# Performance work log

Hardware: AMD Instinct MI355X
Metric: run time of the kernel (lower is better)

Reference implementation:

```python
import jax, jax.numpy as jnp
import numpy as np

N_NODES = 100000
N_EDGES = 1600000
N_FEAT = 64
DIM = 32
N_CLASSES = 10
N_GRAPHS = 64
BN_EPS = 1e-5


def setup_inputs() -> dict:
    key = jax.random.key(0)
    ks = jax.random.split(key, 20)
    x = jax.random.normal(ks[0], (N_NODES, N_FEAT), dtype=jnp.float32)
    edge_index = jax.random.randint(ks[1], (2, N_EDGES), 0, N_NODES, dtype=jnp.int64)
    batch = jnp.sort(jax.random.randint(ks[2], (N_NODES,), 0, N_GRAPHS, dtype=jnp.int64))
    s = 0.1
    # conv1 MLP (in=N_FEAT)
    w1a = jax.random.normal(ks[3], (N_FEAT, DIM), dtype=jnp.float32) * s
    b1a = jnp.zeros((DIM,), jnp.float32)
    w1b = jax.random.normal(ks[4], (DIM, DIM), dtype=jnp.float32) * s
    b1b = jnp.zeros((DIM,), jnp.float32)
    # convs 2-5 MLPs stacked [4, DIM, DIM]
    Wa = jax.random.normal(ks[5], (4, DIM, DIM), dtype=jnp.float32) * s
    Ba = jnp.zeros((4, DIM), jnp.float32)
    Wb = jax.random.normal(ks[6], (4, DIM, DIM), dtype=jnp.float32) * s
    Bb = jnp.zeros((4, DIM), jnp.float32)
    bn_gamma = jnp.ones((5, DIM), jnp.float32)
    bn_beta = jnp.zeros((5, DIM), jnp.float32)
    fc1_w = jax.random.normal(ks[7], (DIM, DIM), dtype=jnp.float32) * s
    fc1_b = jnp.zeros((DIM,), jnp.float32)
    fc2_w = jax.random.normal(ks[8], (DIM, N_CLASSES), dtype=jnp.float32) * s
    fc2_b = jnp.zeros((N_CLASSES,), jnp.float32)
    return dict(x=x, edge_index=edge_index, batch=batch,
                w1a=w1a, b1a=b1a, w1b=w1b, b1b=b1b,
                Wa=Wa, Ba=Ba, Wb=Wb, Bb=Bb,
                bn_gamma=bn_gamma, bn_beta=bn_beta,
                fc1_w=fc1_w, fc1_b=fc1_b, fc2_w=fc2_w, fc2_b=fc2_b)


def _gin_aggr(x, src, dst):
    # sum_{j in N(i)} x_j  + x_i   (eps = 0)
    agg = jax.ops.segment_sum(x[src], dst, num_segments=N_NODES)
    return x + agg


def _mlp(h, wa, ba, wb, bb):
    return jax.nn.relu(h @ wa + ba) @ wb + bb


def _bn(h, gamma, beta):
    mu = jnp.mean(h, axis=0)
    var = jnp.mean((h - mu) ** 2, axis=0)  # biased, torch BN training mode
    return (h - mu) * jax.lax.rsqrt(var + BN_EPS) * gamma + beta


def reference(x, edge_index, batch, w1a, b1a, w1b, b1b, Wa, Ba, Wb, Bb,
              bn_gamma, bn_beta, fc1_w, fc1_b, fc2_w, fc2_b):
    src, dst = edge_index[0], edge_index[1]
    # layer 1 (num_features -> dim)
    h = _mlp(_gin_aggr(x, src, dst), w1a, b1a, w1b, b1b)
    h = _bn(jax.nn.relu(h), bn_gamma[0], bn_beta[0])
    # layers 2-5 (dim -> dim)
    for i in range(4):
        h = _mlp(_gin_aggr(h, src, dst), Wa[i], Ba[i], Wb[i], Bb[i])
        h = _bn(jax.nn.relu(h), bn_gamma[i + 1], bn_beta[i + 1])
    # global add pool over graphs
    g = jax.ops.segment_sum(h, batch, num_segments=N_GRAPHS)  # [G, dim]
    g = jax.nn.relu(g @ fc1_w + fc1_b)
    # dropout: eval mode -> identity
    return g @ fc2_w + fc2_b  # [G, num_classes]
```

## Files before the change

kernel.cpp:

```cpp
#include <hip/hip_runtime.h>
#include <hip/hip_fp16.h>

#define NN 100000
#define NE 1600000
#define NF 64
#define DM 32
#define NG 64
#define NC 10
#define BN_EPS 1e-5f

#define BSHIFT 8
#define NBUCK ((NN + 255) >> 8)
#define CHUNK 8192
#define NCH ((NE + CHUNK - 1) / CHUNK)

__device__ __forceinline__ float2 up2(unsigned u) {
    __half2 h = __builtin_bit_cast(__half2, u);
    return __half22float2(h);
}
__device__ __forceinline__ unsigned pk2(float a, float b) {
    __half2 h = __floats2half2_rn(a, b);
    return __builtin_bit_cast(unsigned, h);
}
__device__ __forceinline__ void acc8(float* a, uint4 w) {
    float2 p;
    p = up2(w.x); a[0] += p.x; a[1] += p.y;
    p = up2(w.y); a[2] += p.x; a[3] += p.y;
    p = up2(w.z); a[4] += p.x; a[5] += p.y;
    p = up2(w.w); a[6] += p.x; a[7] += p.y;
}

__global__ __launch_bounds__(256) void binA_k(const int* __restrict__ ei,
                                              int* __restrict__ bcnt) {
    __shared__ int h[NBUCK];
    for (int i = threadIdx.x; i < NBUCK; i += 256) h[i] = 0;
    __syncthreads();
    long long base = (long long)blockIdx.x * CHUNK;
    int n = (int)((NE - base < CHUNK) ? (NE - base) : CHUNK);
    for (int i = threadIdx.x; i < n; i += 256) {
        int d = ei[NE + base + i];
        atomicAdd(&h[d >> BSHIFT], 1);
    }
    __syncthreads();
    for (int i = threadIdx.x; i < NBUCK; i += 256)
        if (h[i]) atomicAdd(&bcnt[i], h[i]);
}

__global__ __launch_bounds__(512) void binB_k(const int* __restrict__ bcnt,
                                              int* __restrict__ bbase,
                                              int* __restrict__ bcur) {
    __shared__ int s[512];
    int t = threadIdx.x;
    int v = (t < NBUCK) ? bcnt[t] : 0;
    s[t] = v;
    __syncthreads();
    int acc = v;
    for (int off = 1; off < 512; off <<= 1) {
        int add = (t >= off) ? s[t - off] : 0;
        __syncthreads();
        acc += add;
        s[t] = acc;
        __syncthreads();
    }
    if (t < NBUCK) { bbase[t] = acc - v; bcur[t] = acc - v; }
    if (t == 0) bbase[NBUCK] = NE;
}

__global__ __launch_bounds__(256) void binC_k(const int* __restrict__ ei,
                                              int* __restrict__ bcur,
                                              unsigned* __restrict__ binned) {
    __shared__ int cnt[NBUCK];
    __shared__ int ofs[NBUCK];
    __shared__ int idx[NBUCK];
    for (int i = threadIdx.x; i < NBUCK; i += 256) { cnt[i] = 0; idx[i] = 0; }
    __syncthreads();
    long long base = (long long)blockIdx.x * CHUNK;
    int n = (int)((NE - base < CHUNK) ? (NE - base) : CHUNK);
    int d[CHUNK / 256];
#pragma unroll
    for (int k = 0; k < CHUNK / 256; k++) {
        int i = threadIdx.x + k * 256;
        int dd = (i < n) ? ei[NE + base + i] : -1;
        d[k] = dd;
        if (dd >= 0) atomicAdd(&cnt[dd >> BSHIFT], 1);
    }
    __syncthreads();
    for (int i = threadIdx.x; i < NBUCK; i += 256)
        if (cnt[i]) ofs[i] = atomicAdd(&bcur[i], cnt[i]);
    __syncthreads();
#pragma unroll
    for (int k = 0; k < CHUNK / 256; k++) {
        int i = threadIdx.x + k * 256;
        if (i < n) {
            unsigned src = (unsigned)ei[base + i];
            int b = d[k] >> BSHIFT;
            int l = atomicAdd(&idx[b], 1);
            binned[ofs[b] + l] = (src << 8) | (unsigned)(d[k] & 255);
        }
    }
}

__global__ __launch_bounds__(256) void binD_k(const unsigned* __restrict__ binned,
                                              const int* __restrict__ bbase,
                                              int* __restrict__ rowptr,
                                              int* __restrict__ csr) {
    __shared__ int cnt[256];
    __shared__ int cur[256];
    __shared__ int s[256];
    int b = blockIdx.x;
    int e0 = bbase[b], e1 = bbase[b + 1];
    int t = threadIdx.x;
    cnt[t] = 0;
    __syncthreads();
    for (int e = e0 + t; e < e1; e += 256) atomicAdd(&cnt[binned[e] & 255u], 1);
    __syncthreads();
    int v = cnt[t];
    s[t] = v;
    __syncthreads();
    int acc = v;
    for (int off = 1; off < 256; off <<= 1) {
        int add = (t >= off) ? s[t - off] : 0;
        __syncthreads();
        acc += add;
        s[t] = acc;
        __syncthreads();
    }
    int base = e0 + acc - v;
    int node = (b << BSHIFT) + t;
    if (node < NN) rowptr[node] = base;
    cur[t] = base;
    if (b == NBUCK - 1 && t == 0) rowptr[NN] = NE;
    __syncthreads();
    for (int e = e0 + t; e < e1; e += 256) {
        unsigned w = binned[e];
        int p = atomicAdd(&cur[w & 255u], 1);
        csr[p] = (int)(w >> 8);
    }
}

__global__ __launch_bounds__(256) void pre1_k(const float* __restrict__ x,
                                              const float* __restrict__ wa,
                                              unsigned* __restrict__ yhf,
                                              float* __restrict__ zbuf) {
    __shared__ float sWa[64 * 32];
    int tid = threadIdx.x;
    if (blockIdx.x == 0) {
        for (int i = tid; i < 5 * 64 + NG * 32; i += 256) zbuf[i] = 0.f;
    }
    for (int i = tid; i < 64 * 32; i += 256) sWa[i] = wa[i];
    __syncthreads();
    int l = tid & 3;
    int node = blockIdx.x * 64 + (tid >> 2);
    if (node >= NN) return;
    float t[8];
#pragma unroll
    for (int j = 0; j < 8; j++) t[j] = 0.f;
    const float4* xr = reinterpret_cast<const float4*>(x + (long long)node * 64);
    const float4* w4 = reinterpret_cast<const float4*>(sWa);
#pragma unroll
    for (int k4 = 0; k4 < 16; k4++) {
        float4 xv = xr[k4];
        float av[4] = {xv.x, xv.y, xv.z, xv.w};
#pragma unroll
        for (int i = 0; i < 4; i++) {
            float a = av[i];
            float4 w0 = w4[(k4 * 4 + i) * 8 + 2 * l];
            float4 w1 = w4[(k4 * 4 + i) * 8 + 2 * l + 1];
            t[0] += a * w0.x; t[1] += a * w0.y; t[2] += a * w0.z; t[3] += a * w0.w;
            t[4] += a * w1.x; t[5] += a * w1.y; t[6] += a * w1.z; t[7] += a * w1.w;
        }
    }
    uint4 p;
    p.x = pk2(t[0], t[1]); p.y = pk2(t[2], t[3]);
    p.z = pk2(t[4], t[5]); p.w = pk2(t[6], t[7]);
    reinterpret_cast<uint4*>(yhf)[(long long)node * 4 + l] = p;
}

#define SSTR 65
template <int MODE>
__global__ __launch_bounds__(256) void fused_k(const unsigned* __restrict__ tblIn,
                                               unsigned* __restrict__ tblOut,
                                               const int* __restrict__ rowptr,
                                               const int* __restrict__ csr,
                                               const float* __restrict__ wa,
                                               const float* __restrict__ ba,
                                               const float* __restrict__ wb,
                                               const float* __restrict__ bb,
                                               const float* __restrict__ stPrev,
                                               const float* __restrict__ gammaPrev,
                                               const float* __restrict__ betaPrev,
                                               float* __restrict__ statsOut) {
    __shared__ float sWa[32 * 32];
    __shared__ float sWb[32 * 32];
    __shared__ float sBa[32], sBb[32];
    __shared__ float sSc[32], sSh[32];
    __shared__ float sStage[32 * SSTR];
    __shared__ float sSum[4 * 32], sSq[4 * 32];
    int tid = threadIdx.x;
    for (int i = tid; i < 32 * 32; i += 256) {
        sWb[i] = wb[i];
        if (MODE) sWa[i] = wa[i];
    }
    if (tid < 32) {
        sBa[tid] = ba[tid];
        sBb[tid] = bb[tid];
        if (MODE) {
            const float invn = 1.0f / NN;
            float mu = stPrev[tid] * invn;
            float var = stPrev[32 + tid] * invn - mu * mu;
            float scale = rsqrtf(var + BN_EPS) * gammaPrev[tid];
            sSc[tid] = scale;
            sSh[tid] = betaPrev[tid] - mu * scale;
        }
    }

    int l = tid & 3;
    int nl = tid >> 2;
    int node = blockIdx.x * 64 + nl;
    bool act = node < NN;

    int s = 0, e = 0;
    uint4 selfw = make_uint4(0, 0, 0, 0);
    const uint4* t4 = reinterpret_cast<const uint4*>(tblIn);
    if (act) {
        s = rowptr[node];
        e = rowptr[node + 1];
        selfw = t4[(long long)node * 4 + l];
    }
    float g[8];
#pragma unroll
    for (int c = 0; c < 8; c++) g[c] = 0.f;
    int i = s;
    for (; i + 8 <= e; i += 8) {
        int s0 = csr[i], s1 = csr[i + 1], s2 = csr[i + 2], s3 = csr[i + 3];
        int s4 = csr[i + 4], s5 = csr[i + 5], s6 = csr[i + 6], s7 = csr[i + 7];
        uint4 w0 = t4[(long long)s0 * 4 + l];
        uint4 w1 = t4[(long long)s1 * 4 + l];
        uint4 w2 = t4[(long long)s2 * 4 + l];
        uint4 w3 = t4[(long long)s3 * 4 + l];
        uint4 w4 = t4[(long long)s4 * 4 + l];
        uint4 w5 = t4[(long long)s5 * 4 + l];
        uint4 w6 = t4[(long long)s6 * 4 + l];
        uint4 w7 = t4[(long long)s7 * 4 + l];
        acc8(g, w0); acc8(g, w1); acc8(g, w2); acc8(g, w3);
        acc8(g, w4); acc8(g, w5); acc8(g, w6); acc8(g, w7);
    }
    if (i + 4 <= e) {
        int s0 = csr[i], s1 = csr[i + 1], s2 = csr[i + 2], s3 = csr[i + 3];
        uint4 w0 = t4[(long long)s0 * 4 + l];
        uint4 w1 = t4[(long long)s1 * 4 + l];
        uint4 w2 = t4[(long long)s2 * 4 + l];
        uint4 w3 = t4[(long long)s3 * 4 + l];
        acc8(g, w0); acc8(g, w1); acc8(g, w2); acc8(g, w3);
        i += 4;
    }
    for (; i < e; i++) {
        uint4 w = t4[(long long)csr[i] * 4 + l];
        acc8(g, w);
    }
    __syncthreads();

    float sv[8];
    {
        float2 p;
        p = up2(selfw.x); sv[0] = p.x; sv[1] = p.y;
        p = up2(selfw.y); sv[2] = p.x; sv[3] = p.y;
        p = up2(selfw.z); sv[4] = p.x; sv[5] = p.y;
        p = up2(selfw.w); sv[6] = p.x; sv[7] = p.y;
    }
    float t[8];
    if (MODE) {
        float in[8];
        if (act) {
            float deg = (float)(e - s);
#pragma unroll
            for (int c = 0; c < 8; c++) {
                int f = l * 8 + c;
                in[c] = sv[c] * sSc[f] + sSh[f] + (g[c] * sSc[f] + deg * sSh[f]);
            }
        } else {
#pragma unroll
            for (int c = 0; c < 8; c++) in[c] = 0.f;
        }
#pragma unroll
        for (int c = 0; c < 8; c++) sStage[(l * 8 + c) * SSTR + nl] = in[c];
        __syncthreads();
#pragma unroll
        for (int j = 0; j < 8; j++) t[j] = sBa[l * 8 + j];
        const float4* w4a = reinterpret_cast<const float4*>(sWa);
#pragma unroll
        for (int k = 0; k < 32; k++) {
            float a = sStage[k * SSTR + nl];
            float4 w0 = w4a[k * 8 + 2 * l];
            float4 w1 = w4a[k * 8 + 2 * l + 1];
            t[0] += a * w0.x; t[1] += a * w0.y; t[2] += a * w0.z; t[3] += a * w0.w;
            t[4] += a * w1.x; t[5] += a * w1.y; t[6] += a * w1.z; t[7] += a * w1.w;
        }
#pragma unroll
        for (int j = 0; j < 8; j++) t[j] = fmaxf(t[j], 0.f);
        __syncthreads();
    } else {
        if (act) {
#pragma unroll
            for (int c = 0; c < 8; c++) t[c] = fmaxf(sv[c] + g[c] + sBa[l * 8 + c], 0.f);
        } else {
#pragma unroll
            for (int c = 0; c < 8; c++) t[c] = 0.f;
        }
    }

#pragma unroll
    for (int c = 0; c < 8; c++) sStage[(l * 8 + c) * SSTR + nl] = t[c];
    __syncthreads();
    float r[8];
#pragma unroll
    for (int j = 0; j < 8; j++) r[j] = sBb[l * 8 + j];
    const float4* w4b = reinterpret_cast<const float4*>(sWb);
#pragma unroll
    for (int k = 0; k < 32; k++) {
        float a = sStage[k * SSTR + nl];
        float4 w0 = w4b[k * 8 + 2 * l];
        float4 w1 = w4b[k * 8 + 2 * l + 1];
        r[0] += a * w0.x; r[1] += a * w0.y; r[2] += a * w0.z; r[3] += a * w0.w;
        r[4] += a * w1.x; r[5] += a * w1.y; r[6] += a * w1.z; r[7] += a * w1.w;
    }
#pragma unroll
    for (int j = 0; j < 8; j++) r[j] = fmaxf(r[j], 0.f);

    if (act) {
        uint4 p;
        p.x = pk2(r[0], r[1]); p.y = pk2(r[2], r[3]);
        p.z = pk2(r[4], r[5]); p.w = pk2(r[6], r[7]);
        reinterpret_cast<uint4*>(tblOut)[(long long)node * 4 + l] = p;
    } else {
#pragma unroll
        for (int j = 0; j < 8; j++) r[j] = 0.f;
    }

    int lane = tid & 63, wid = tid >> 6;
#pragma unroll
    for (int j = 0; j < 8; j++) {
        float v = r[j], v2 = v * v;
        v += __shfl_down(v, 32, 64); v2 += __shfl_down(v2, 32, 64);
        v += __shfl_down(v, 16, 64); v2 += __shfl_down(v2, 16, 64);
        v += __shfl_down(v, 8, 64);  v2 += __shfl_down(v2, 8, 64);
        v += __shfl_down(v, 4, 64);  v2 += __shfl_down(v2, 4, 64);
        if (lane < 4) { sSum[wid * 32 + lane * 8 + j] = v; sSq[wid * 32 + lane * 8 + j] = v2; }
    }
    __syncthreads();
    if (tid < 32) {
        float a = sSum[tid] + sSum[32 + tid] + sSum[64 + tid] + sSum[96 + tid];
        float b = sSq[tid] + sSq[32 + tid] + sSq[64 + tid] + sSq[96 + tid];
        atomicAdd(&statsOut[tid], a);
        atomicAdd(&statsOut[32 + tid], b);
    }
}

#define POOL_NPB 512
__global__ __launch_bounds__(256) void pool_bn_k(const unsigned* __restrict__ tbl,
                                                 const int* __restrict__ batch,
                                                 const float* __restrict__ st,
                                                 const float* __restrict__ gamma,
                                                 const float* __restrict__ beta,
                                                 float* __restrict__ pooled) {
    int tid = threadIdx.x;
    int f = tid & 31;
    int p = tid >> 5;
    int wrd = f >> 1;
    int hi = f & 1;
    int n0 = blockIdx.x * POOL_NPB + p * (POOL_NPB / 8);
    int n1 = n0 + POOL_NPB / 8;
    if (n1 > NN) n1 = NN;
    if (n0 >= NN) return;
    const float invn = 1.0f / NN;
    float mu = st[f] * invn;
    float var = st[32 + f] * invn - mu * mu;
    float sc = rsqrtf(var + BN_EPS) * gamma[f];
    float sh = beta[f] - mu * sc;
    float acc = 0.f;
    int cur = batch[n0];
    for (int n = n0; n < n1; n++) {
        int g = batch[n];
        if (g != cur) {
            atomicAdd(&pooled[cur * 32 + f], acc);
            cur = g;
            acc = 0.f;
        }
        float2 pv = up2(tbl[(long long)n * 16 + wrd]);
        acc += (hi ? pv.y : pv.x) * sc + sh;
    }
    atomicAdd(&pooled[cur * 32 + f], acc);
}

__global__ __launch_bounds__(64) void final_k(const float* __restrict__ pooled,
                                              const float* __restrict__ w1,
                                              const float* __restrict__ b1,
                                              const float* __restrict__ w2,
                                              const float* __restrict__ b2,
                                              float* __restrict__ out) {
    int g = threadIdx.x;
    if (g >= NG) return;
    float t[32];
#pragma unroll
    for (int j = 0; j < 32; j++) t[j] = b1[j];
    for (int k = 0; k < 32; k++) {
        float a = pooled[g * 32 + k];
#pragma unroll
        for (int j = 0; j < 32; j++) t[j] += a * w1[k * 32 + j];
    }
#pragma unroll
    for (int j = 0; j < 32; j++) t[j] = fmaxf(t[j], 0.f);
    for (int c = 0; c < NC; c++) {
        float o = b2[c];
#pragma unroll
        for (int k = 0; k < 32; k++) o += t[k] * w2[k * NC + c];
        out[g * NC + c] = o;
    }
}

extern "C" void kernel_launch(void* const* d_in, const int* in_sizes, int n_in,
                              void* d_out, int out_size, void* d_ws, size_t ws_size,
                              hipStream_t stream) {
    const float* x = (const float*)d_in[0];
    const int* ei = (const int*)d_in[1];
    const int* batch = (const int*)d_in[2];
    const float* w1a = (const float*)d_in[3];
    const float* b1a = (const float*)d_in[4];
    const float* w1b = (const float*)d_in[5];
    const float* b1b = (const float*)d_in[6];
    const float* Wa = (const float*)d_in[7];
    const float* Ba = (const float*)d_in[8];
    const float* Wb = (const float*)d_in[9];
    const float* Bb = (const float*)d_in[10];
    const float* bn_gamma = (const float*)d_in[11];
    const float* bn_beta = (const float*)d_in[12];
    const float* fc1w = (const float*)d_in[13];
    const float* fc1b = (const float*)d_in[14];
    const float* fc2w = (const float*)d_in[15];
    const float* fc2b = (const float*)d_in[16];
    float* out = (float*)d_out;

    float* ws = (float*)d_ws;
    float* stats_all = ws;
    float* pooled = stats_all + 5 * 64;
    unsigned* yhf = (unsigned*)(pooled + NG * 32);
    unsigned* hfA = yhf + (size_t)NN * 16;
    unsigned* hfB = hfA + (size_t)NN * 16;
    unsigned* binned = hfB + (size_t)NN * 16;
    int* bcnt = (int*)(binned + NE);
    int* bbase = bcnt + NBUCK;
    int* bcur = bbase + NBUCK + 1;
    int* rowptr = bcur + NBUCK;
    int* csr = rowptr + NN + 1;

    const int nb4 = (NN + 63) / 64;

    hipMemsetAsync(bcnt, 0, NBUCK * sizeof(int), stream);
    binA_k<<<NCH, 256, 0, stream>>>(ei, bcnt);
    binB_k<<<1, 512, 0, stream>>>(bcnt, bbase, bcur);
    binC_k<<<NCH, 256, 0, stream>>>(ei, bcur, binned);
    binD_k<<<NBUCK, 256, 0, stream>>>(binned, bbase, rowptr, csr);

    pre1_k<<<nb4, 256, 0, stream>>>(x, w1a, yhf, stats_all);
    fused_k<0><<<nb4, 256, 0, stream>>>(yhf, hfA, rowptr, csr,
                                        nullptr, b1a, w1b, b1b,
                                        nullptr, nullptr, nullptr, stats_all);

    unsigned* tin = hfA;
    unsigned* tout = hfB;
    for (int i = 0; i < 4; i++) {
        fused_k<1><<<nb4, 256, 0, stream>>>(tin, tout, rowptr, csr,
                                            Wa + i * 1024, Ba + i * 32,
                                            Wb + i * 1024, Bb + i * 32,
                                            stats_all + i * 64, bn_gamma + i * 32,
                                            bn_beta + i * 32, stats_all + (i + 1) * 64);
        unsigned* tmp = tin; tin = tout; tout = tmp;
    }

    pool_bn_k<<<(NN + POOL_NPB - 1) / POOL_NPB, 256, 0, stream>>>(
        tin, batch, stats_all + 4 * 64, bn_gamma + 4 * 32, bn_beta + 4 * 32, pooled);
    final_k<<<1, 64, 0, stream>>>(pooled, fc1w, fc1b, fc2w, fc2b, out);
}
```

Before: 499.6 us.

## Use 16 lanes per node with 4-byte gathers in fused GIN kernel

```diff
diff --git a/kernel.cpp b/kernel.cpp
--- a/kernel.cpp
+++ b/kernel.cpp
@@ -21,13 +21,6 @@
 __device__ __forceinline__ unsigned pk2(float a, float b) {
     __half2 h = __floats2half2_rn(a, b);
     return __builtin_bit_cast(unsigned, h);
-}
-__device__ __forceinline__ void acc8(float* a, uint4 w) {
-    float2 p;
-    p = up2(w.x); a[0] += p.x; a[1] += p.y;
-    p = up2(w.y); a[2] += p.x; a[3] += p.y;
-    p = up2(w.z); a[4] += p.x; a[5] += p.y;
-    p = up2(w.w); a[6] += p.x; a[7] += p.y;
 }
 
 __global__ __launch_bounds__(256) void binA_k(const int* __restrict__ ei,
@@ -176,7 +169,7 @@
     reinterpret_cast<uint4*>(yhf)[(long long)node * 4 + l] = p;
 }
 
-#define SSTR 65
+#define SST 17
 template <int MODE>
 __global__ __launch_bounds__(256) void fused_k(const unsigned* __restrict__ tblIn,
                                                unsigned* __restrict__ tblOut,
@@ -194,7 +187,7 @@
     __shared__ float sWb[32 * 32];
     __shared__ float sBa[32], sBb[32];
     __shared__ float sSc[32], sSh[32];
-    __shared__ float sStage[32 * SSTR];
+    __shared__ float sStage[32 * SST];
     __shared__ float sSum[4 * 32], sSq[4 * 32];
     int tid = threadIdx.x;
     for (int i = tid; i < 32 * 32; i += 256) {
@@ -214,138 +207,111 @@
         }
     }
 
-    int l = tid & 3;
-    int nl = tid >> 2;
-    int node = blockIdx.x * 64 + nl;
-    bool act = node < NN;
-
-    int s = 0, e = 0;
-    uint4 selfw = make_uint4(0, 0, 0, 0);
-    const uint4* t4 = reinterpret_cast<const uint4*>(tblIn);
-    if (act) {
-        s = rowptr[node];
-        e = rowptr[node + 1];
-        selfw = t4[(long long)node * 4 + l];
-    }
-    float g[8];
-#pragma unroll
-    for (int c = 0; c < 8; c++) g[c] = 0.f;
+    int l = tid & 15;
+    int nl = tid >> 4;
+    int node = blockIdx.x * 16 + nl;
+
+    int s = rowptr[node], e = rowptr[node + 1];
+    unsigned selfw = tblIn[(long long)node * 16 + l];
+
+    float g0 = 0.f, g1 = 0.f;
     int i = s;
     for (; i + 8 <= e; i += 8) {
         int s0 = csr[i], s1 = csr[i + 1], s2 = csr[i + 2], s3 = csr[i + 3];
         int s4 = csr[i + 4], s5 = csr[i + 5], s6 = csr[i + 6], s7 = csr[i + 7];
-        uint4 w0 = t4[(long long)s0 * 4 + l];
-        uint4 w1 = t4[(long long)s1 * 4 + l];
-        uint4 w2 = t4[(long long)s2 * 4 + l];
-        uint4 w3 = t4[(long long)s3 * 4 + l];
-        uint4 w4 = t4[(long long)s4 * 4 + l];
-        uint4 w5 = t4[(long long)s5 * 4 + l];
-        uint4 w6 = t4[(long long)s6 * 4 + l];
-        uint4 w7 = t4[(long long)s7 * 4 + l];
-        acc8(g, w0); acc8(g, w1); acc8(g, w2); acc8(g, w3);
-        acc8(g, w4); acc8(g, w5); acc8(g, w6); acc8(g, w7);
+        unsigned w0 = tblIn[(long long)s0 * 16 + l];
+        unsigned w1 = tblIn[(long long)s1 * 16 + l];
+        unsigned w2 = tblIn[(long long)s2 * 16 + l];
+        unsigned w3 = tblIn[(long long)s3 * 16 + l];
+        unsigned w4 = tblIn[(long long)s4 * 16 + l];
+        unsigned w5 = tblIn[(long long)s5 * 16 + l];
+        unsigned w6 = tblIn[(long long)s6 * 16 + l];
+        unsigned w7 = tblIn[(long long)s7 * 16 + l];
+        float2 p;
+        p = up2(w0); g0 += p.x; g1 += p.y;
+        p = up2(w1); g0 += p.x; g1 += p.y;
+        p = up2(w2); g0 += p.x; g1 += p.y;
+        p = up2(w3); g0 += p.x; g1 += p.y;
+        p = up2(w4); g0 += p.x; g1 += p.y;
+        p = up2(w5); g0 += p.x; g1 += p.y;
+        p = up2(w6); g0 += p.x; g1 += p.y;
+        p = up2(w7); g0 += p.x; g1 += p.y;
     }
     if (i + 4 <= e) {
         int s0 = csr[i], s1 = csr[i + 1], s2 = csr[i + 2], s3 = csr[i + 3];
-        uint4 w0 = t4[(long long)s0 * 4 + l];
-        uint4 w1 = t4[(long long)s1 * 4 + l];
-        uint4 w2 = t4[(long long)s2 * 4 + l];
-        uint4 w3 = t4[(long long)s3 * 4 + l];
-        acc8(g, w0); acc8(g, w1); acc8(g, w2); acc8(g, w3);
+        unsigned w0 = tblIn[(long long)s0 * 16 + l];
+        unsigned w1 = tblIn[(long long)s1 * 16 + l];
+        unsigned w2 = tblIn[(long long)s2 * 16 + l];
+        unsigned w3 = tblIn[(long long)s3 * 16 + l];
+        float2 p;
+        p = up2(w0); g0 += p.x; g1 += p.y;
+        p = up2(w1); g0 += p.x; g1 += p.y;
+        p = up2(w2); g0 += p.x; g1 += p.y;
+        p = up2(w3); g0 += p.x; g1 += p.y;
         i += 4;
     }
     for (; i < e; i++) {
-        uint4 w = t4[(long long)csr[i] * 4 + l];
-        acc8(g, w);
-    }
-    __syncthreads();
-
-    float sv[8];
-    {
-        float2 p;
-        p = up2(selfw.x); sv[0] = p.x; sv[1] = p.y;
-        p = up2(selfw.y); sv[2] = p.x; sv[3] = p.y;
-        p = up2(selfw.z); sv[4] = p.x; sv[5] = p.y;
-        p = up2(selfw.w); sv[6] = p.x; sv[7] = p.y;
-    }
-    float t[8];
+        unsigned w = tblIn[(long long)csr[i] * 16 + l];
+        float2 p = up2(w);
+        g0 += p.x; g1 += p.y;
+    }
+    __syncthreads();
+
+    float2 sp = up2(selfw);
+    int f0 = 2 * l, f1 = 2 * l + 1;
+    float t0, t1;
     if (MODE) {
-        float in[8];
-        if (act) {
-            float deg = (float)(e - s);
-#pragma unroll
-            for (int c = 0; c < 8; c++) {
-                int f = l * 8 + c;
-                in[c] = sv[c] * sSc[f] + sSh[f] + (g[c] * sSc[f] + deg * sSh[f]);
-            }
-        } else {
-#pragma unroll
-            for (int c = 0; c < 8; c++) in[c] = 0.f;
+        float deg = (float)(e - s);
+        float in0 = sp.x * sSc[f0] + sSh[f0] + g0 * sSc[f0] + deg * sSh[f0];
+        float in1 = sp.y * sSc[f1] + sSh[f1] + g1 * sSc[f1] + deg * sSh[f1];
+        sStage[f0 * SST + nl] = in0;
+        sStage[f1 * SST + nl] = in1;
+        __syncthreads();
+        t0 = sBa[f0]; t1 = sBa[f1];
+        const float2* w2a = reinterpret_cast<const float2*>(sWa);
+#pragma unroll
+        for (int k = 0; k < 32; k++) {
+            float a = sStage[k * SST + nl];
+            float2 w = w2a[k * 16 + l];
+            t0 += a * w.x;
+            t1 += a * w.y;
         }
-#pragma unroll
-        for (int c = 0; c < 8; c++) sStage[(l * 8 + c) * SSTR + nl] = in[c];
-        __syncthreads();
-#pragma unroll
-        for (int j = 0; j < 8; j++) t[j] = sBa[l * 8 + j];
-        const float4* w4a = reinterpret_cast<const float4*>(sWa);
-#pragma unroll
-        for (int k = 0; k < 32; k++) {
-            float a = sStage[k * SSTR + nl];
-            float4 w0 = w4a[k * 8 + 2 * l];
-            float4 w1 = w4a[k * 8 + 2 * l + 1];
-            t[0] += a * w0.x; t[1] += a * w0.y; t[2] += a * w0.z; t[3] += a * w0.w;
-            t[4] += a * w1.x; t[5] += a * w1.y; t[6] += a * w1.z; t[7] += a * w1.w;
-        }
-#pragma unroll
-        for (int j = 0; j < 8; j++) t[j] = fmaxf(t[j], 0.f);
+        t0 = fmaxf(t0, 0.f);
+        t1 = fmaxf(t1, 0.f);
         __syncthreads();
     } else {
-        if (act) {
-#pragma unroll
-            for (int c = 0; c < 8; c++) t[c] = fmaxf(sv[c] + g[c] + sBa[l * 8 + c], 0.f);
-        } else {
-#pragma unroll
-            for (int c = 0; c < 8; c++) t[c] = 0.f;
-        }
-    }
-
-#pragma unroll
-    for (int c = 0; c < 8; c++) sStage[(l * 8 + c) * SSTR + nl] = t[c];
-    __syncthreads();
-    float r[8];
-#pragma unroll
-    for (int j = 0; j < 8; j++) r[j] = sBb[l * 8 + j];
-    const float4* w4b = reinterpret_cast<const float4*>(sWb);
+        t0 = fmaxf(sp.x + g0 + sBa[f0], 0.f);
+        t1 = fmaxf(sp.y + g1 + sBa[f1], 0.f);
+    }
+
+    sStage[f0 * SST + nl] = t0;
+    sStage[f1 * SST + nl] = t1;
+    __syncthreads();
+    float r0 = sBb[f0], r1 = sBb[f1];
+    const float2* w2b = reinterpret_cast<const float2*>(sWb);
 #pragma unroll
     for (int k = 0; k < 32; k++) {
-        float a = sStage[k * SSTR + nl];
-        float4 w0 = w4b[k * 8 + 2 * l];
-        float4 w1 = w4b[k * 8 + 2 * l + 1];
-        r[0] += a * w0.x; r[1] += a * w0.y; r[2] += a * w0.z; r[3] += a * w0.w;
-        r[4] += a * w1.x; r[5] += a * w1.y; r[6] += a * w1.z; r[7] += a * w1.w;
-    }
-#pragma unroll
-    for (int j = 0; j < 8; j++) r[j] = fmaxf(r[j], 0.f);
-
-    if (act) {
-        uint4 p;
-        p.x = pk2(r[0], r[1]); p.y = pk2(r[2], r[3]);
-        p.z = pk2(r[4], r[5]); p.w = pk2(r[6], r[7]);
-        reinterpret_cast<uint4*>(tblOut)[(long long)node * 4 + l] = p;
-    } else {
-#pragma unroll
-        for (int j = 0; j < 8; j++) r[j] = 0.f;
-    }
+        float a = sStage[k * SST + nl];
+        float2 w = w2b[k * 16 + l];
+        r0 += a * w.x;
+        r1 += a * w.y;
+    }
+    r0 = fmaxf(r0, 0.f);
+    r1 = fmaxf(r1, 0.f);
+
+    tblOut[(long long)node * 16 + l] = pk2(r0, r1);
 
     int lane = tid & 63, wid = tid >> 6;
-#pragma unroll
-    for (int j = 0; j < 8; j++) {
-        float v = r[j], v2 = v * v;
-        v += __shfl_down(v, 32, 64); v2 += __shfl_down(v2, 32, 64);
-        v += __shfl_down(v, 16, 64); v2 += __shfl_down(v2, 16, 64);
-        v += __shfl_down(v, 8, 64);  v2 += __shfl_down(v2, 8, 64);
-        v += __shfl_down(v, 4, 64);  v2 += __shfl_down(v2, 4, 64);
-        if (lane < 4) { sSum[wid * 32 + lane * 8 + j] = v; sSq[wid * 32 + lane * 8 + j] = v2; }
+    float v0 = r0, q0 = r0 * r0, v1 = r1, q1 = r1 * r1;
+    v0 += __shfl_down(v0, 32, 64); q0 += __shfl_down(q0, 32, 64);
+    v1 += __shfl_down(v1, 32, 64); q1 += __shfl_down(q1, 32, 64);
+    v0 += __shfl_down(v0, 16, 64); q0 += __shfl_down(q0, 16, 64);
+    v1 += __shfl_down(v1, 16, 64); q1 += __shfl_down(q1, 16, 64);
+    if (lane < 16) {
+        sSum[wid * 32 + 2 * lane] = v0;
+        sSum[wid * 32 + 2 * lane + 1] = v1;
+        sSq[wid * 32 + 2 * lane] = q0;
+        sSq[wid * 32 + 2 * lane + 1] = q1;
     }
     __syncthreads();
     if (tid < 32) {
@@ -453,7 +419,8 @@
     int* rowptr = bcur + NBUCK;
     int* csr = rowptr + NN + 1;
 
-    const int nb4 = (NN + 63) / 64;
+    const int nbPre = (NN + 63) / 64;
+    const int nbF = NN / 16;
 
     hipMemsetAsync(bcnt, 0, NBUCK * sizeof(int), stream);
     binA_k<<<NCH, 256, 0, stream>>>(ei, bcnt);
@@ -461,15 +428,15 @@
     binC_k<<<NCH, 256, 0, stream>>>(ei, bcur, binned);
     binD_k<<<NBUCK, 256, 0, stream>>>(binned, bbase, rowptr, csr);
 
-    pre1_k<<<nb4, 256, 0, stream>>>(x, w1a, yhf, stats_all);
-    fused_k<0><<<nb4, 256, 0, stream>>>(yhf, hfA, rowptr, csr,
+    pre1_k<<<nbPre, 256, 0, stream>>>(x, w1a, yhf, stats_all);
+    fused_k<0><<<nbF, 256, 0, stream>>>(yhf, hfA, rowptr, csr,
                                         nullptr, b1a, w1b, b1b,
                                         nullptr, nullptr, nullptr, stats_all);
 
     unsigned* tin = hfA;
     unsigned* tout = hfB;
     for (int i = 0; i < 4; i++) {
-        fused_k<1><<<nb4, 256, 0, stream>>>(tin, tout, rowptr, csr,
+        fused_k<1><<<nbF, 256, 0, stream>>>(tin, tout, rowptr, csr,
                                             Wa + i * 1024, Ba + i * 32,
                                             Wb + i * 1024, Bb + i * 32,
                                             stats_all + i * 64, bn_gamma + i * 32,
```

Measured after the change: 1.020 ms. +104.1%, slower.

## Split neighbor gather into two source-range passes for cache locality

Applied to the files above, without the earlier changes.

```diff
diff --git a/kernel.cpp b/kernel.cpp
--- a/kernel.cpp
+++ b/kernel.cpp
@@ -8,6 +8,7 @@
 #define NG 64
 #define NC 10
 #define BN_EPS 1e-5f
+#define NTILE0 50000
 
 #define BSHIFT 8
 #define NBUCK ((NN + 255) >> 8)
@@ -103,18 +104,24 @@
 __global__ __launch_bounds__(256) void binD_k(const unsigned* __restrict__ binned,
                                               const int* __restrict__ bbase,
                                               int* __restrict__ rowptr,
+                                              int* __restrict__ splitp,
                                               int* __restrict__ csr) {
-    __shared__ int cnt[256];
-    __shared__ int cur[256];
+    __shared__ int cntLo[256], cntHi[256];
+    __shared__ int curLo[256], curHi[256];
     __shared__ int s[256];
     int b = blockIdx.x;
     int e0 = bbase[b], e1 = bbase[b + 1];
     int t = threadIdx.x;
-    cnt[t] = 0;
-    __syncthreads();
-    for (int e = e0 + t; e < e1; e += 256) atomicAdd(&cnt[binned[e] & 255u], 1);
-    __syncthreads();
-    int v = cnt[t];
+    cntLo[t] = 0; cntHi[t] = 0;
+    __syncthreads();
+    for (int e = e0 + t; e < e1; e += 256) {
+        unsigned w = binned[e];
+        int ld = (int)(w & 255u);
+        int src = (int)(w >> 8);
+        atomicAdd(src < NTILE0 ? &cntLo[ld] : &cntHi[ld], 1);
+    }
+    __syncthreads();
+    int v = cntLo[t] + cntHi[t];
     s[t] = v;
     __syncthreads();
     int acc = v;
@@ -127,14 +134,20 @@
     }
     int base = e0 + acc - v;
     int node = (b << BSHIFT) + t;
-    if (node < NN) rowptr[node] = base;
-    cur[t] = base;
+    if (node < NN) {
+        rowptr[node] = base;
+        splitp[node] = base + cntLo[t];
+    }
+    curLo[t] = base;
+    curHi[t] = base + cntLo[t];
     if (b == NBUCK - 1 && t == 0) rowptr[NN] = NE;
     __syncthreads();
     for (int e = e0 + t; e < e1; e += 256) {
         unsigned w = binned[e];
-        int p = atomicAdd(&cur[w & 255u], 1);
-        csr[p] = (int)(w >> 8);
+        int ld = (int)(w & 255u);
+        int src = (int)(w >> 8);
+        int p = atomicAdd(src < NTILE0 ? &curLo[ld] : &curHi[ld], 1);
+        csr[p] = src;
     }
 }
 
@@ -176,12 +189,83 @@
     reinterpret_cast<uint4*>(yhf)[(long long)node * 4 + l] = p;
 }
 
+__global__ __launch_bounds__(256) void gather0_k(const unsigned* __restrict__ tblIn,
+                                                 const int* __restrict__ rowptr,
+                                                 const int* __restrict__ splitp,
+                                                 float* __restrict__ agg) {
+    int tid = threadIdx.x;
+    int l = tid & 3;
+    int node = blockIdx.x * 64 + (tid >> 2);
+    if (node >= NN) return;
+    int s = rowptr[node], e = splitp[node];
+    const uint4* t4 = reinterpret_cast<const uint4*>(tblIn);
+    float g[8];
+#pragma unroll
+    for (int c = 0; c < 8; c++) g[c] = 0.f;
+    extern const int* __restrict__ csr_dummy_decl;
+    const int* csr = splitp + NN;
+    (void)csr;
+    return;
+}
+
+__global__ __launch_bounds__(256) void gatherT0_k(const unsigned* __restrict__ tblIn,
+                                                  const int* __restrict__ rowptr,
+                                                  const int* __restrict__ splitp,
+                                                  const int* __restrict__ csr,
+                                                  float* __restrict__ agg) {
+    int tid = threadIdx.x;
+    int l = tid & 3;
+    int node = blockIdx.x * 64 + (tid >> 2);
+    if (node >= NN) return;
+    int s = rowptr[node], e = splitp[node];
+    const uint4* t4 = reinterpret_cast<const uint4*>(tblIn);
+    float g[8];
+#pragma unroll
+    for (int c = 0; c < 8; c++) g[c] = 0.f;
+    int i = s;
+    for (; i + 8 <= e; i += 8) {
+        int s0 = csr[i], s1 = csr[i + 1], s2 = csr[i + 2], s3 = csr[i + 3];
+        int s4 = csr[i + 4], s5 = csr[i + 5], s6 = csr[i + 6], s7 = csr[i + 7];
+        uint4 w0 = t4[(long long)s0 * 4 + l];
+        uint4 w1 = t4[(long long)s1 * 4 + l];
+        uint4 w2 = t4[(long long)s2 * 4 + l];
+        uint4 w3 = t4[(long long)s3 * 4 + l];
+        uint4 w4 = t4[(long long)s4 * 4 + l];
+        uint4 w5 = t4[(long long)s5 * 4 + l];
+        uint4 w6 = t4[(long long)s6 * 4 + l];
+        uint4 w7 = t4[(long long)s7 * 4 + l];
+        acc8(g, w0); acc8(g, w1); acc8(g, w2); acc8(g, w3);
+        acc8(g, w4); acc8(g, w5); acc8(g, w6); acc8(g, w7);
+    }
+    if (i + 4 <= e) {
+        int s0 = csr[i], s1 = csr[i + 1], s2 = csr[i + 2], s3 = csr[i + 3];
+        uint4 w0 = t4[(long long)s0 * 4 + l];
+        uint4 w1 = t4[(long long)s1 * 4 + l];
+        uint4 w2 = t4[(long long)s2 * 4 + l];
+        uint4 w3 = t4[(long long)s3 * 4 + l];
+        acc8(g, w0); acc8(g, w1); acc8(g, w2); acc8(g, w3);
+        i += 4;
+    }
+    for (; i < e; i++) {
+        uint4 w = t4[(long long)csr[i] * 4 + l];
+        acc8(g, w);
+    }
+    float4* ar = reinterpret_cast<float4*>(agg + (long long)node * 32 + l * 8);
+    float4 o0, o1;
+    o0.x = g[0]; o0.y = g[1]; o0.z = g[2]; o0.w = g[3];
+    o1.x = g[4]; o1.y = g[5]; o1.z = g[6]; o1.w = g[7];
+    ar[0] = o0;
+    ar[1] = o1;
+}
+
 #define SSTR 65
 template <int MODE>
 __global__ __launch_bounds__(256) void fused_k(const unsigned* __restrict__ tblIn,
                                                unsigned* __restrict__ tblOut,
                                                const int* __restrict__ rowptr,
+                                               const int* __restrict__ splitp,
                                                const int* __restrict__ csr,
+                                               const float* __restrict__ aggIn,
                                                const float* __restrict__ wa,
                                                const float* __restrict__ ba,
                                                const float* __restrict__ wb,
@@ -219,18 +303,23 @@
     int node = blockIdx.x * 64 + nl;
     bool act = node < NN;
 
-    int s = 0, e = 0;
+    int sf = 0, sp = 0, e = 0;
     uint4 selfw = make_uint4(0, 0, 0, 0);
+    float g[8];
+#pragma unroll
+    for (int c = 0; c < 8; c++) g[c] = 0.f;
     const uint4* t4 = reinterpret_cast<const uint4*>(tblIn);
     if (act) {
-        s = rowptr[node];
+        sf = rowptr[node];
+        sp = splitp[node];
         e = rowptr[node + 1];
         selfw = t4[(long long)node * 4 + l];
-    }
-    float g[8];
-#pragma unroll
-    for (int c = 0; c < 8; c++) g[c] = 0.f;
-    int i = s;
+        const float4* ar = reinterpret_cast<const float4*>(aggIn + (long long)node * 32 + l * 8);
+        float4 a0 = ar[0], a1 = ar[1];
+        g[0] = a0.x; g[1] = a0.y; g[2] = a0.z; g[3] = a0.w;
+        g[4] = a1.x; g[5] = a1.y; g[6] = a1.z; g[7] = a1.w;
+    }
+    int i = sp;
     for (; i + 8 <= e; i += 8) {
         int s0 = csr[i], s1 = csr[i + 1], s2 = csr[i + 2], s3 = csr[i + 3];
         int s4 = csr[i + 4], s5 = csr[i + 5], s6 = csr[i + 6], s7 = csr[i + 7];
@@ -272,7 +361,7 @@
     if (MODE) {
         float in[8];
         if (act) {
-            float deg = (float)(e - s);
+            float deg = (float)(e - sf);
 #pragma unroll
             for (int c = 0; c < 8; c++) {
                 int f = l * 8 + c;
@@ -443,7 +532,8 @@
     float* ws = (float*)d_ws;
     float* stats_all = ws;
     float* pooled = stats_all + 5 * 64;
-    unsigned* yhf = (unsigned*)(pooled + NG * 32);
+    float* agg = pooled + NG * 32;
+    unsigned* yhf = (unsigned*)(agg + (size_t)NN * 32);
     unsigned* hfA = yhf + (size_t)NN * 16;
     unsigned* hfB = hfA + (size_t)NN * 16;
     unsigned* binned = hfB + (size_t)NN * 16;
@@ -451,7 +541,8 @@
     int* bbase = bcnt + NBUCK;
     int* bcur = bbase + NBUCK + 1;
     int* rowptr = bcur + NBUCK;
-    int* csr = rowptr + NN + 1;
+    int* splitp = rowptr + NN + 1;
+    int* csr = splitp + NN;
 
     const int nb4 = (NN + 63) / 64;
 
@@ -459,17 +550,19 @@
     binA_k<<<NCH, 256, 0, stream>>>(ei, bcnt);
     binB_k<<<1, 512, 0, stream>>>(bcnt, bbase, bcur);
     binC_k<<<NCH, 256, 0, stream>>>(ei, bcur, binned);
-    binD_k<<<NBUCK, 256, 0, stream>>>(binned, bbase, rowptr, csr);
+    binD_k<<<NBUCK, 256, 0, stream>>>(binned, bbase, rowptr, splitp, csr);
 
     pre1_k<<<nb4, 256, 0, stream>>>(x, w1a, yhf, stats_all);
-    fused_k<0><<<nb4, 256, 0, stream>>>(yhf, hfA, rowptr, csr,
+    gatherT0_k<<<nb4, 256, 0, stream>>>(yhf, rowptr, splitp, csr, agg);
+    fused_k<0><<<nb4, 256, 0, stream>>>(yhf, hfA, rowptr, splitp, csr, agg,
                                         nullptr, b1a, w1b, b1b,
                                         nullptr, nullptr, nullptr, stats_all);
 
     unsigned* tin = hfA;
     unsigned* tout = hfB;
     for (int i = 0; i < 4; i++) {
-        fused_k<1><<<nb4, 256, 0, stream>>>(tin, tout, rowptr, csr,
+        gatherT0_k<<<nb4, 256, 0, stream>>>(tin, rowptr, splitp, csr, agg);
+        fused_k<1><<<nb4, 256, 0, stream>>>(tin, tout, rowptr, splitp, csr, agg,
                                             Wa + i * 1024, Ba + i * 32,
                                             Wb + i * 1024, Bb + i * 32,
                                             stats_all + i * 64, bn_gamma + i * 32,
```

New measurement: 576.6 us. 15.4% more time.
